# Kernel optimization log

Hardware: AMD Instinct MI355X
Metric: run time of the kernel (lower is better)

Reference implementation:

```python
import jax, jax.numpy as jnp
import numpy as np

B, S, D, P = 16, 128, 768, 1024
N_CLASSES = 121  # dataset != 'restaurant'


def setup_inputs() -> dict:
    key = jax.random.key(0)
    ks = jax.random.split(key, 8)
    scale = lambda fan_in: 1.0 / np.sqrt(fan_in)
    return {
        "spans_embedding": jax.random.normal(ks[0], (B, S, D), dtype=jnp.float32),
        "W1": jax.random.normal(ks[1], (3 * D, 2 * D), dtype=jnp.float32) * scale(3 * D),
        "b1": jnp.zeros((2 * D,), dtype=jnp.float32),
        "W2": jax.random.normal(ks[2], (2 * D, D), dtype=jnp.float32) * scale(2 * D),
        "b2": jnp.zeros((D,), dtype=jnp.float32),
        "W3": jax.random.normal(ks[3], (D, N_CLASSES), dtype=jnp.float32) * scale(D),
        "b3": jnp.zeros((N_CLASSES,), dtype=jnp.float32),
        "span_masks": jnp.ones((B, S), dtype=jnp.int32),
        "batch_idx": jax.random.randint(ks[4], (P,), 0, B, dtype=jnp.int64),
        "aspect_idx": jax.random.randint(ks[5], (P,), 0, S - 2, dtype=jnp.int64),
        "opinion_idx": jax.random.randint(ks[6], (P,), 0, S - 2, dtype=jnp.int64),
    }


def reference(spans_embedding, W1, b1, W2, b2, W3, b3,
              span_masks, batch_idx, aspect_idx, opinion_idx):
    S_ = spans_embedding.shape[1]
    pos = jnp.arange(S_)
    last = jnp.sum(span_masks, axis=1) - 1          # [B] last valid span index
    li = last[batch_idx]                             # [P]
    emb = spans_embedding[batch_idx]                 # [P, S, D] gathered per pair

    def rng_max(lo, hi):                             # max over spans in [lo, hi)
        mask = (pos[None, :] >= lo[:, None]) & (pos[None, :] < hi[:, None])
        return jnp.max(jnp.where(mask[:, :, None], emb, -jnp.inf), axis=1)

    def rng_mean(lo, hi):                            # mean over spans in [lo, hi)
        m = ((pos[None, :] >= lo[:, None]) & (pos[None, :] < hi[:, None])).astype(emb.dtype)
        cnt = jnp.maximum(jnp.sum(m, axis=1), 1.0)
        return jnp.einsum('ps,psd->pd', m, emb) / cnt[:, None]

    ones = jnp.ones_like(aspect_idx)
    # boundary index b: aspect when aspect!=0, else opinion (matches all non-both-zero branches)
    b = jnp.where(aspect_idx != 0, aspect_idx, opinion_idx)
    emb0 = spans_embedding[batch_idx, 0]             # [P, D]
    embL = spans_embedding[batch_idx, li]            # [P, D]
    left_nz = jnp.where((b == 1)[:, None], emb0, rng_max(ones, b))
    right_nz = jnp.where((b == li)[:, None], embL, rng_max(b, li))

    both0 = (aspect_idx == 0) & (opinion_idx == 0)
    left = jnp.where(both0[:, None], rng_mean(ones, li), left_nz)
    right = jnp.where(both0[:, None], rng_max(ones, li), right_nz)

    aspect_rep = spans_embedding[batch_idx, aspect_idx]
    o_eff = jnp.where(opinion_idx == 0, li, opinion_idx)
    opinion_rep = spans_embedding[batch_idx, o_eff]

    x = jnp.concatenate([aspect_rep + opinion_rep, left, right], axis=1)  # [P, 3D]
    h = jax.nn.relu(x @ W1 + b1)
    h = jax.nn.relu(h @ W2 + b2)
    return h @ W3 + b3                               # [P, n_classes]
```

## Files before the change

### kernel.cpp

```cpp
#include <hip/hip_runtime.h>
#include <hip/hip_bf16.h>
#include <math.h>

#define S_LEN 128
#define D_DIM 768
#define P_PAIRS 1024
#define B_BATCH 16

typedef __attribute__((ext_vector_type(8))) short bf16x8;
typedef __attribute__((ext_vector_type(4))) float f32x4;

#define PB_UNITS (B_BATCH * (D_DIM / 64))
#define T1_UNITS ((2304 / 64) * (1536 / 64))
#define T2_UNITS ((1536 / 64) * (768 / 64))
#define T3_UNITS ((768 / 64) * (128 / 64))

union SmemU {
    struct {
        ushort semb[128][64];
        ushort spref[128][64];
        ushort ssuf[128][64];
        ushort smean[64];
        float  lred[3][4][64];
        int    li;
    } pb;
    float t64[64][65];
};

__device__ __forceinline__ ushort f2bf(float f) {
    __hip_bfloat16 h = __float2bfloat16(f);
    return *(ushort*)&h;
}

__device__ __forceinline__ float bf2f(ushort u) {
    unsigned int x = ((unsigned int)u) << 16;
    float f;
    __builtin_memcpy(&f, &x, 4);
    return f;
}

__device__ __forceinline__ void gload16(const void* g, void* l) {
    __builtin_amdgcn_global_load_lds(
        (const __attribute__((address_space(1))) void*)g,
        (__attribute__((address_space(3))) void*)l, 16, 0, 0);
}

__global__ __launch_bounds__(256) void fused_prep_kernel(
    const float* __restrict__ emb_all,
    const int* __restrict__ span_masks,
    const int* __restrict__ batch_idx,
    const int* __restrict__ aspect_idx,
    const int* __restrict__ opinion_idx,
    ushort* __restrict__ X,
    const float* __restrict__ W1, ushort* __restrict__ W1t,
    const float* __restrict__ W2, ushort* __restrict__ W2t,
    const float* __restrict__ W3, ushort* __restrict__ W3t)
{
    __shared__ SmemU sm;
    __shared__ int wsum[4];
    int bid = blockIdx.x;
    int tid = threadIdx.x;

    if (bid < PB_UNITS) {
        int b = bid / (D_DIM / 64);
        int chunk = bid % (D_DIM / 64);
        int lane = tid & 63;
        int g = tid >> 6;
        int r0 = g * 32;
        int col = chunk * 64 + lane;

        {
            int mv = (tid < S_LEN) ? span_masks[b * S_LEN + tid] : 0;
            #pragma unroll
            for (int off = 32; off > 0; off >>= 1)
                mv += __shfl_down(mv, off);
            if (lane == 0) wsum[g] = mv;
            __syncthreads();
            if (tid == 0) sm.pb.li = wsum[0] + wsum[1] + wsum[2] + wsum[3] - 1;
            __syncthreads();
        }
        int li = sm.pb.li;

        const float* embb = emb_all + (size_t)b * S_LEN * D_DIM;

        float v[32];
        #pragma unroll
        for (int r = 0; r < 32; ++r) {
            v[r] = embb[(size_t)(r0 + r) * D_DIM + col];
            sm.pb.semb[r0 + r][lane] = f2bf(v[r]);
        }

        float wmax = -INFINITY, umax = -INFINITY, s = 0.f;
        #pragma unroll
        for (int r = 0; r < 32; ++r) {
            int gr = r0 + r;
            wmax = fmaxf(wmax, (gr == 0) ? -INFINITY : v[r]);
            bool in = (gr >= 1) && (gr < li);
            umax = fmaxf(umax, in ? v[r] : -INFINITY);
            s += in ? v[r] : 0.f;
        }
        sm.pb.lred[0][g][lane] = wmax;
        sm.pb.lred[1][g][lane] = umax;
        sm.pb.lred[2][g][lane] = s;
        __syncthreads();

        float basep = -INFINITY;
        #pragma unroll
        for (int gg = 0; gg < 3; ++gg)
            if (gg < g) basep = fmaxf(basep, sm.pb.lred[0][gg][lane]);
        float bases = -INFINITY;
        #pragma unroll
        for (int gg = 1; gg < 4; ++gg)
            if (gg > g) bases = fmaxf(bases, sm.pb.lred[1][gg][lane]);

        if (g == 0) {
            float tot = sm.pb.lred[2][0][lane] + sm.pb.lred[2][1][lane]
                      + sm.pb.lred[2][2][lane] + sm.pb.lred[2][3][lane];
            int cnt = (li - 1) > 0 ? (li - 1) : 1;
            sm.pb.smean[lane] = f2bf(tot / (float)cnt);
        }

        float m = basep;
        #pragma unroll
        for (int r = 0; r < 32; ++r) {
            int gr = r0 + r;
            m = fmaxf(m, (gr == 0) ? -INFINITY : v[r]);
            sm.pb.spref[gr][lane] = f2bf(m);
        }
        float m2 = bases;
        #pragma unroll
        for (int r = 31; r >= 0; --r) {
            int gr = r0 + r;
            bool in = (gr >= 1) && (gr < li);
            m2 = fmaxf(m2, in ? v[r] : -INFINITY);
            if (gr >= 1) sm.pb.ssuf[gr][lane] = f2bf(m2);
        }
        __syncthreads();

        int pbase = g * 256;
        for (int c = 0; c < 256; c += 64) {
            int p = pbase + c + lane;
            int vb = batch_idx[p];
            int va = aspect_idx[p];
            int vo = opinion_idx[p];
            unsigned long long mask = __ballot(vb == b);
            while (mask) {
                int i = __ffsll((long long)mask) - 1;
                mask &= mask - 1;
                int pp = pbase + c + i;
                int a = __shfl(va, i);
                int o = __shfl(vo, i);
                bool both0 = (a == 0) && (o == 0);
                int bnd = (a != 0) ? a : o;
                int oe = (o == 0) ? li : o;
                float ar  = bf2f(sm.pb.semb[a][lane]);
                float orp = bf2f(sm.pb.semb[oe][lane]);
                ushort left, right;
                if (both0) {
                    left  = sm.pb.smean[lane];
                    right = sm.pb.spref[li - 1][lane];
                } else {
                    left  = (bnd == 1)  ? sm.pb.semb[0][lane]
                                        : sm.pb.spref[bnd - 1][lane];
                    right = (bnd == li) ? sm.pb.semb[li][lane]
                                        : sm.pb.ssuf[bnd][lane];
                }
                size_t base = (size_t)pp * (3 * D_DIM) + col;
                X[base]             = f2bf(ar + orp);
                X[base + D_DIM]     = left;
                X[base + 2 * D_DIM] = right;
            }
        }
    } else {
        int tb = bid - PB_UNITS;
        const float* in; ushort* out; int K, N, Npad, bx, by;
        if (tb < T1_UNITS) {
            in = W1; out = W1t; K = 2304; N = 1536; Npad = 1536;
            bx = tb % (2304 / 64); by = tb / (2304 / 64);
        } else if (tb < T1_UNITS + T2_UNITS) {
            tb -= T1_UNITS;
            in = W2; out = W2t; K = 1536; N = 768; Npad = 768;
            bx = tb % (1536 / 64); by = tb / (1536 / 64);
        } else {
            tb -= T1_UNITS + T2_UNITS;
            in = W3; out = W3t; K = 768; N = 121; Npad = 128;
            bx = tb % (768 / 64); by = tb / (768 / 64);
        }
        int k0 = bx * 64, n0 = by * 64;

        int kr = tid >> 2;
        int nq = (tid & 3) * 16;
        if (n0 + 64 <= N) {
            #pragma unroll
            for (int j = 0; j < 4; ++j) {
                float4 vv = *(const float4*)&in[(size_t)(k0 + kr) * N + n0 + nq + j * 4];
                *(float4*)&sm.t64[kr][nq + j * 4] = vv;
            }
        } else {
            #pragma unroll
            for (int j = 0; j < 16; ++j) {
                int n = n0 + nq + j;
                sm.t64[kr][nq + j] = (n < N) ? in[(size_t)(k0 + kr) * N + n] : 0.f;
            }
        }
        __syncthreads();

        int nr = tid >> 2;
        int kq = (tid & 3) * 16;
        if (n0 + nr < Npad) {
            ushort tmp[16];
            #pragma unroll
            for (int j = 0; j < 16; ++j) tmp[j] = f2bf(sm.t64[kq + j][nr]);
            ushort* dst = out + (size_t)(n0 + nr) * K + k0 + kq;
            *(bf16x8*)dst       = *(bf16x8*)&tmp[0];
            *(bf16x8*)(dst + 8) = *(bf16x8*)&tmp[8];
        }
    }
}

template<int WRITE_BF16, int RELU>
__global__ __launch_bounds__(256, 2) void gemm_mfma(
    const ushort* __restrict__ A,
    const ushort* __restrict__ Bt,
    const float* __restrict__ bias,
    void* __restrict__ Cout,
    int M, int N, int K)
{
    __shared__ ushort lds[4][128 * 64];
    int tid = threadIdx.x;
    int lane = tid & 63;
    int w = tid >> 6;
    int wr = w >> 1, wc = w & 1;
    int rowBase = blockIdx.y * 64;
    int colBase = blockIdx.x * 64;

    int srow  = lane >> 3;
    int scolb = (((lane & 7) ^ srow) << 4);
    const char* Abase = (const char*)(A  + (size_t)rowBase * K);
    const char* Bbase = (const char*)(Bt + (size_t)colBase * K);
    size_t rstride = (size_t)K * 2;

    f32x4 acc[2][2] = {};
    int nt = K >> 6;

    auto stage = [&](int buf, int t) {
        size_t kb0 = (size_t)t << 7;
        #pragma unroll
        for (int i = 0; i < 2; ++i) {
            int r = w * 16 + i * 8 + srow;
            gload16(Abase + (size_t)r * rstride + kb0 + scolb,
                    &lds[buf][(w * 16 + i * 8) * 64]);
        }
        #pragma unroll
        for (int i = 0; i < 2; ++i) {
            int r = w * 16 + i * 8 + srow;
            gload16(Bbase + (size_t)r * rstride + kb0 + scolb,
                    &lds[buf][(64 + w * 16 + i * 8) * 64]);
        }
    };

    stage(0, 0);
    stage(1, 1);
    stage(2, 2);

    for (int t = 0; t < nt; ++t) {
        int cur = t & 3;
        int ahead = nt - 1 - t;
        if (ahead >= 2)      asm volatile("s_waitcnt vmcnt(8)" ::: "memory");
        else if (ahead == 1) asm volatile("s_waitcnt vmcnt(4)" ::: "memory");
        else                 asm volatile("s_waitcnt vmcnt(0)" ::: "memory");
        __builtin_amdgcn_s_barrier();
        __builtin_amdgcn_sched_barrier(0);

        if (t + 3 < nt) stage((t + 3) & 3, t + 3);

        const char* lb = (const char*)&lds[cur][0];
        int kq = (lane >> 4) << 4;
        bf16x8 af[2][2], bfr[2][2];
        #pragma unroll
        for (int m = 0; m < 2; ++m) {
            int row = wr * 32 + m * 16 + (lane & 15);
            #pragma unroll
            for (int kk = 0; kk < 2; ++kk) {
                int addr = row * 128 + ((kq + kk * 64) ^ ((row & 7) << 4));
                af[m][kk] = *(const bf16x8*)(lb + addr);
            }
        }
        #pragma unroll
        for (int n = 0; n < 2; ++n) {
            int row = 64 + wc * 32 + n * 16 + (lane & 15);
            #pragma unroll
            for (int kk = 0; kk < 2; ++kk) {
                int addr = row * 128 + ((kq + kk * 64) ^ ((row & 7) << 4));
                bfr[n][kk] = *(const bf16x8*)(lb + addr);
            }
        }
        __builtin_amdgcn_s_setprio(1);
        #pragma unroll
        for (int m = 0; m < 2; ++m)
            #pragma unroll
            for (int n = 0; n < 2; ++n)
                #pragma unroll
                for (int kk = 0; kk < 2; ++kk)
                    acc[m][n] = __builtin_amdgcn_mfma_f32_16x16x32_bf16(
                        af[m][kk], bfr[n][kk], acc[m][n], 0, 0, 0);
        __builtin_amdgcn_s_setprio(0);
    }

    #pragma unroll
    for (int m = 0; m < 2; ++m) {
        #pragma unroll
        for (int n = 0; n < 2; ++n) {
            #pragma unroll
            for (int j = 0; j < 4; ++j) {
                int row = rowBase + wr * 32 + m * 16 + (lane >> 4) * 4 + j;
                int col = colBase + wc * 32 + n * 16 + (lane & 15);
                if (col < N && row < M) {
                    float v = acc[m][n][j] + bias[col];
                    if (RELU) v = fmaxf(v, 0.f);
                    if (WRITE_BF16)
                        ((ushort*)Cout)[(size_t)row * N + col] = f2bf(v);
                    else
                        ((float*)Cout)[(size_t)row * N + col] = v;
                }
            }
        }
    }
}

extern "C" void kernel_launch(void* const* d_in, const int* in_sizes, int n_in,
                              void* d_out, int out_size, void* d_ws, size_t ws_size,
                              hipStream_t stream) {
    const float* emb        = (const float*)d_in[0];
    const float* W1         = (const float*)d_in[1];
    const float* b1         = (const float*)d_in[2];
    const float* W2         = (const float*)d_in[3];
    const float* b2         = (const float*)d_in[4];
    const float* W3         = (const float*)d_in[5];
    const float* b3         = (const float*)d_in[6];
    const int* span_masks   = (const int*)d_in[7];
    const int* batch_idx    = (const int*)d_in[8];
    const int* aspect_idx   = (const int*)d_in[9];
    const int* opinion_idx  = (const int*)d_in[10];
    float* out = (float*)d_out;

    ushort* Xb  = (ushort*)d_ws;
    ushort* H2  = Xb;
    ushort* W1t = Xb  + (size_t)1024 * 2304;
    ushort* W2t = W1t + (size_t)1536 * 2304;
    ushort* W3t = W2t + (size_t)768 * 1536;
    ushort* H1  = W3t + (size_t)128 * 768;

    fused_prep_kernel<<<PB_UNITS + T1_UNITS + T2_UNITS + T3_UNITS, 256, 0, stream>>>(
        emb, span_masks, batch_idx, aspect_idx, opinion_idx, Xb,
        W1, W1t, W2, W2t, W3, W3t);

    gemm_mfma<1,1><<<dim3(1536/64, 1024/64), 256, 0, stream>>>(Xb, W1t, b1, H1, 1024, 1536, 2304);
    gemm_mfma<1,1><<<dim3( 768/64, 1024/64), 256, 0, stream>>>(H1, W2t, b2, H2, 1024, 768, 1536);
    gemm_mfma<0,0><<<dim3( 128/64, 1024/64), 256, 0, stream>>>(H2, W3t, b3, out, 1024, 121, 768);
}
```

Measured before the change: 54.10 us.

## Split prep kernel and overlap W2/W3 transposes with first GEMM

The single fused prep launch is split into a span-feature kernel and a separate W1 transpose kernel. The W2 and W3 transpose blocks are appended to the first GEMM's grid so they run alongside the GEMM tiles instead of before them. The aim is to shorten the serial prep phase by moving work the first GEMM does not need off its critical path. The cost is one extra launch and a GEMM1 kernel whose shared memory is a union sized by the GEMM buffers.

```diff
diff --git a/kernel.cpp b/kernel.cpp
--- a/kernel.cpp
+++ b/kernel.cpp
@@ -14,17 +14,20 @@
 #define T1_UNITS ((2304 / 64) * (1536 / 64))
 #define T2_UNITS ((1536 / 64) * (768 / 64))
 #define T3_UNITS ((768 / 64) * (128 / 64))
-
-union SmemU {
-    struct {
-        ushort semb[128][64];
-        ushort spref[128][64];
-        ushort ssuf[128][64];
-        ushort smean[64];
-        float  lred[3][4][64];
-        int    li;
-    } pb;
-    float t64[64][65];
+#define G1_TILES (24 * 16)
+
+struct SmemPB {
+    ushort semb[128][64];
+    ushort spref[128][64];
+    ushort ssuf[128][64];
+    ushort smean[64];
+    float  lred[3][4][64];
+    int    li;
+};
+
+union GSmem {
+    ushort lds[4][128 * 64];
+    float  t64[64][65];
 };
 
 __device__ __forceinline__ ushort f2bf(float f) {
@@ -43,6 +46,41 @@
     __builtin_amdgcn_global_load_lds(
         (const __attribute__((address_space(1))) void*)g,
         (__attribute__((address_space(3))) void*)l, 16, 0, 0);
+}
+
+__device__ __forceinline__ void transpose_unit(
+    float (*t64)[65], const float* __restrict__ in, ushort* __restrict__ out,
+    int K, int N, int Npad, int bx, int by, int tid)
+{
+    int k0 = bx * 64, n0 = by * 64;
+
+    int kr = tid >> 2;
+    int nq = (tid & 3) * 16;
+    if (n0 + 64 <= N) {
+        #pragma unroll
+        for (int j = 0; j < 4; ++j) {
+            float4 vv = *(const float4*)&in[(size_t)(k0 + kr) * N + n0 + nq + j * 4];
+            *(float4*)&t64[kr][nq + j * 4] = vv;
+        }
+    } else {
+        #pragma unroll
+        for (int j = 0; j < 16; ++j) {
+            int n = n0 + nq + j;
+            t64[kr][nq + j] = (n < N) ? in[(size_t)(k0 + kr) * N + n] : 0.f;
+        }
+    }
+    __syncthreads();
+
+    int nr = tid >> 2;
+    int kq = (tid & 3) * 16;
+    if (n0 + nr < Npad) {
+        ushort tmp[16];
+        #pragma unroll
+        for (int j = 0; j < 16; ++j) tmp[j] = f2bf(t64[kq + j][nr]);
+        ushort* dst = out + (size_t)(n0 + nr) * K + k0 + kq;
+        *(bf16x8*)dst       = *(bf16x8*)&tmp[0];
+        *(bf16x8*)(dst + 8) = *(bf16x8*)&tmp[8];
+    }
 }
 
 __global__ __launch_bounds__(256) void fused_prep_kernel(
@@ -51,169 +89,247 @@
     const int* __restrict__ batch_idx,
     const int* __restrict__ aspect_idx,
     const int* __restrict__ opinion_idx,
-    ushort* __restrict__ X,
-    const float* __restrict__ W1, ushort* __restrict__ W1t,
+    ushort* __restrict__ X)
+{
+    __shared__ SmemPB sm;
+    __shared__ int wsum[4];
+    int bid = blockIdx.x;
+    int tid = threadIdx.x;
+
+    int b = bid / (D_DIM / 64);
+    int chunk = bid % (D_DIM / 64);
+    int lane = tid & 63;
+    int g = tid >> 6;
+    int r0 = g * 32;
+    int col = chunk * 64 + lane;
+
+    {
+        int mv = (tid < S_LEN) ? span_masks[b * S_LEN + tid] : 0;
+        #pragma unroll
+        for (int off = 32; off > 0; off >>= 1)
+            mv += __shfl_down(mv, off);
+        if (lane == 0) wsum[g] = mv;
+        __syncthreads();
+        if (tid == 0) sm.li = wsum[0] + wsum[1] + wsum[2] + wsum[3] - 1;
+        __syncthreads();
+    }
+    int li = sm.li;
+
+    const float* embb = emb_all + (size_t)b * S_LEN * D_DIM;
+
+    float v[32];
+    #pragma unroll
+    for (int r = 0; r < 32; ++r) {
+        v[r] = embb[(size_t)(r0 + r) * D_DIM + col];
+        sm.semb[r0 + r][lane] = f2bf(v[r]);
+    }
+
+    float wmax = -INFINITY, umax = -INFINITY, s = 0.f;
+    #pragma unroll
+    for (int r = 0; r < 32; ++r) {
+        int gr = r0 + r;
+        wmax = fmaxf(wmax, (gr == 0) ? -INFINITY : v[r]);
+        bool in = (gr >= 1) && (gr < li);
+        umax = fmaxf(umax, in ? v[r] : -INFINITY);
+        s += in ? v[r] : 0.f;
+    }
+    sm.lred[0][g][lane] = wmax;
+    sm.lred[1][g][lane] = umax;
+    sm.lred[2][g][lane] = s;
+    __syncthreads();
+
+    float basep = -INFINITY;
+    #pragma unroll
+    for (int gg = 0; gg < 3; ++gg)
+        if (gg < g) basep = fmaxf(basep, sm.lred[0][gg][lane]);
+    float bases = -INFINITY;
+    #pragma unroll
+    for (int gg = 1; gg < 4; ++gg)
+        if (gg > g) bases = fmaxf(bases, sm.lred[1][gg][lane]);
+
+    if (g == 0) {
+        float tot = sm.lred[2][0][lane] + sm.lred[2][1][lane]
+                  + sm.lred[2][2][lane] + sm.lred[2][3][lane];
+        int cnt = (li - 1) > 0 ? (li - 1) : 1;
+        sm.smean[lane] = f2bf(tot / (float)cnt);
+    }
+
+    float m = basep;
+    #pragma unroll
+    for (int r = 0; r < 32; ++r) {
+        int gr = r0 + r;
+        m = fmaxf(m, (gr == 0) ? -INFINITY : v[r]);
+        sm.spref[gr][lane] = f2bf(m);
+    }
+    float m2 = bases;
+    #pragma unroll
+    for (int r = 31; r >= 0; --r) {
+        int gr = r0 + r;
+        bool in = (gr >= 1) && (gr < li);
+        m2 = fmaxf(m2, in ? v[r] : -INFINITY);
+        if (gr >= 1) sm.ssuf[gr][lane] = f2bf(m2);
+    }
+    __syncthreads();
+
+    int pbase = g * 256;
+    for (int c = 0; c < 256; c += 64) {
+        int p = pbase + c + lane;
+        int vb = batch_idx[p];
+        int va = aspect_idx[p];
+        int vo = opinion_idx[p];
+        unsigned long long mask = __ballot(vb == b);
+        while (mask) {
+            int i = __ffsll((long long)mask) - 1;
+            mask &= mask - 1;
+            int pp = pbase + c + i;
+            int a = __shfl(va, i);
+            int o = __shfl(vo, i);
+            bool both0 = (a == 0) && (o == 0);
+            int bnd = (a != 0) ? a : o;
+            int oe = (o == 0) ? li : o;
+            float ar  = bf2f(sm.semb[a][lane]);
+            float orp = bf2f(sm.semb[oe][lane]);
+            ushort left, right;
+            if (both0) {
+                left  = sm.smean[lane];
+                right = sm.spref[li - 1][lane];
+            } else {
+                left  = (bnd == 1)  ? sm.semb[0][lane]
+                                    : sm.spref[bnd - 1][lane];
+                right = (bnd == li) ? sm.semb[li][lane]
+                                    : sm.ssuf[bnd][lane];
+            }
+            size_t base = (size_t)pp * (3 * D_DIM) + col;
+            X[base]             = f2bf(ar + orp);
+            X[base + D_DIM]     = left;
+            X[base + 2 * D_DIM] = right;
+        }
+    }
+}
+
+__global__ __launch_bounds__(256) void w1_transpose_kernel(
+    const float* __restrict__ W1, ushort* __restrict__ W1t)
+{
+    __shared__ float t64[64][65];
+    int tb = blockIdx.x;
+    transpose_unit(t64, W1, W1t, 2304, 1536, 1536, tb % 36, tb / 36, threadIdx.x);
+}
+
+__global__ __launch_bounds__(256, 2) void gemm1_plus_t23(
+    const ushort* __restrict__ A,
+    const ushort* __restrict__ Bt,
+    const float* __restrict__ bias,
+    ushort* __restrict__ Cout,
     const float* __restrict__ W2, ushort* __restrict__ W2t,
     const float* __restrict__ W3, ushort* __restrict__ W3t)
 {
-    __shared__ SmemU sm;
-    __shared__ int wsum[4];
+    constexpr int M = 1024, N = 1536, K = 2304;
+    __shared__ GSmem gs;
     int bid = blockIdx.x;
     int tid = threadIdx.x;
 
-    if (bid < PB_UNITS) {
-        int b = bid / (D_DIM / 64);
-        int chunk = bid % (D_DIM / 64);
-        int lane = tid & 63;
-        int g = tid >> 6;
-        int r0 = g * 32;
-        int col = chunk * 64 + lane;
-
-        {
-            int mv = (tid < S_LEN) ? span_masks[b * S_LEN + tid] : 0;
-            #pragma unroll
-            for (int off = 32; off > 0; off >>= 1)
-                mv += __shfl_down(mv, off);
-            if (lane == 0) wsum[g] = mv;
-            __syncthreads();
-            if (tid == 0) sm.pb.li = wsum[0] + wsum[1] + wsum[2] + wsum[3] - 1;
-            __syncthreads();
-        }
-        int li = sm.pb.li;
-
-        const float* embb = emb_all + (size_t)b * S_LEN * D_DIM;
-
-        float v[32];
-        #pragma unroll
-        for (int r = 0; r < 32; ++r) {
-            v[r] = embb[(size_t)(r0 + r) * D_DIM + col];
-            sm.pb.semb[r0 + r][lane] = f2bf(v[r]);
-        }
-
-        float wmax = -INFINITY, umax = -INFINITY, s = 0.f;
-        #pragma unroll
-        for (int r = 0; r < 32; ++r) {
-            int gr = r0 + r;
-            wmax = fmaxf(wmax, (gr == 0) ? -INFINITY : v[r]);
-            bool in = (gr >= 1) && (gr < li);
-            umax = fmaxf(umax, in ? v[r] : -INFINITY);
-            s += in ? v[r] : 0.f;
-        }
-        sm.pb.lred[0][g][lane] = wmax;
-        sm.pb.lred[1][g][lane] = umax;
-        sm.pb.lred[2][g][lane] = s;
-        __syncthreads();
-
-        float basep = -INFINITY;
-        #pragma unroll
-        for (int gg = 0; gg < 3; ++gg)
-            if (gg < g) basep = fmaxf(basep, sm.pb.lred[0][gg][lane]);
-        float bases = -INFINITY;
-        #pragma unroll
-        for (int gg = 1; gg < 4; ++gg)
-            if (gg > g) bases = fmaxf(bases, sm.pb.lred[1][gg][lane]);
-
-        if (g == 0) {
-            float tot = sm.pb.lred[2][0][lane] + sm.pb.lred[2][1][lane]
-                      + sm.pb.lred[2][2][lane] + sm.pb.lred[2][3][lane];
-            int cnt = (li - 1) > 0 ? (li - 1) : 1;
-            sm.pb.smean[lane] = f2bf(tot / (float)cnt);
-        }
-
-        float m = basep;
-        #pragma unroll
-        for (int r = 0; r < 32; ++r) {
-            int gr = r0 + r;
-            m = fmaxf(m, (gr == 0) ? -INFINITY : v[r]);
-            sm.pb.spref[gr][lane] = f2bf(m);
-        }
-        float m2 = bases;
-        #pragma unroll
-        for (int r = 31; r >= 0; --r) {
-            int gr = r0 + r;
-            bool in = (gr >= 1) && (gr < li);
-            m2 = fmaxf(m2, in ? v[r] : -INFINITY);
-            if (gr >= 1) sm.pb.ssuf[gr][lane] = f2bf(m2);
-        }
-        __syncthreads();
-
-        int pbase = g * 256;
-        for (int c = 0; c < 256; c += 64) {
-            int p = pbase + c + lane;
-            int vb = batch_idx[p];
-            int va = aspect_idx[p];
-            int vo = opinion_idx[p];
-            unsigned long long mask = __ballot(vb == b);
-            while (mask) {
-                int i = __ffsll((long long)mask) - 1;
-                mask &= mask - 1;
-                int pp = pbase + c + i;
-                int a = __shfl(va, i);
-                int o = __shfl(vo, i);
-                bool both0 = (a == 0) && (o == 0);
-                int bnd = (a != 0) ? a : o;
-                int oe = (o == 0) ? li : o;
-                float ar  = bf2f(sm.pb.semb[a][lane]);
-                float orp = bf2f(sm.pb.semb[oe][lane]);
-                ushort left, right;
-                if (both0) {
-                    left  = sm.pb.smean[lane];
-                    right = sm.pb.spref[li - 1][lane];
-                } else {
-                    left  = (bnd == 1)  ? sm.pb.semb[0][lane]
-                                        : sm.pb.spref[bnd - 1][lane];
-                    right = (bnd == li) ? sm.pb.semb[li][lane]
-                                        : sm.pb.ssuf[bnd][lane];
-                }
-                size_t base = (size_t)pp * (3 * D_DIM) + col;
-                X[base]             = f2bf(ar + orp);
-                X[base + D_DIM]     = left;
-                X[base + 2 * D_DIM] = right;
-            }
-        }
-    } else {
-        int tb = bid - PB_UNITS;
-        const float* in; ushort* out; int K, N, Npad, bx, by;
-        if (tb < T1_UNITS) {
-            in = W1; out = W1t; K = 2304; N = 1536; Npad = 1536;
-            bx = tb % (2304 / 64); by = tb / (2304 / 64);
-        } else if (tb < T1_UNITS + T2_UNITS) {
-            tb -= T1_UNITS;
-            in = W2; out = W2t; K = 1536; N = 768; Npad = 768;
-            bx = tb % (1536 / 64); by = tb / (1536 / 64);
-        } else {
-            tb -= T1_UNITS + T2_UNITS;
-            in = W3; out = W3t; K = 768; N = 121; Npad = 128;
-            bx = tb % (768 / 64); by = tb / (768 / 64);
-        }
-        int k0 = bx * 64, n0 = by * 64;
-
-        int kr = tid >> 2;
-        int nq = (tid & 3) * 16;
-        if (n0 + 64 <= N) {
+    if (bid >= G1_TILES) {
+        int tb = bid - G1_TILES;
+        if (tb < T2_UNITS)
+            transpose_unit(gs.t64, W2, W2t, 1536, 768, 768, tb % 24, tb / 24, tid);
+        else {
+            tb -= T2_UNITS;
+            transpose_unit(gs.t64, W3, W3t, 768, 121, 128, tb % 12, tb / 12, tid);
+        }
+        return;
+    }
+
+    int lane = tid & 63;
+    int w = tid >> 6;
+    int wr = w >> 1, wc = w & 1;
+    int bx = bid % 24, by = bid / 24;
+    int rowBase = by * 64;
+    int colBase = bx * 64;
+
+    int srow  = lane >> 3;
+    int scolb = (((lane & 7) ^ srow) << 4);
+    const char* Abase = (const char*)(A  + (size_t)rowBase * K);
+    const char* Bbase = (const char*)(Bt + (size_t)colBase * K);
+    size_t rstride = (size_t)K * 2;
+
+    f32x4 acc[2][2] = {};
+    int nt = K >> 6;
+
+    auto stage = [&](int buf, int t) {
+        size_t kb0 = (size_t)t << 7;
+        #pragma unroll
+        for (int i = 0; i < 2; ++i) {
+            int r = w * 16 + i * 8 + srow;
+            gload16(Abase + (size_t)r * rstride + kb0 + scolb,
+                    &gs.lds[buf][(w * 16 + i * 8) * 64]);
+        }
+        #pragma unroll
+        for (int i = 0; i < 2; ++i) {
+            int r = w * 16 + i * 8 + srow;
+            gload16(Bbase + (size_t)r * rstride + kb0 + scolb,
+                    &gs.lds[buf][(64 + w * 16 + i * 8) * 64]);
+        }
+    };
+
+    stage(0, 0);
+    stage(1, 1);
+    stage(2, 2);
+
+    for (int t = 0; t < nt; ++t) {
+        int cur = t & 3;
+        int ahead = nt - 1 - t;
+        if (ahead >= 2)      asm volatile("s_waitcnt vmcnt(8)" ::: "memory");
+        else if (ahead == 1) asm volatile("s_waitcnt vmcnt(4)" ::: "memory");
+        else                 asm volatile("s_waitcnt vmcnt(0)" ::: "memory");
+        __builtin_amdgcn_s_barrier();
+        __builtin_amdgcn_sched_barrier(0);
+
+        if (t + 3 < nt) stage((t + 3) & 3, t + 3);
+
+        const char* lb = (const char*)&gs.lds[cur][0];
+        int kq = (lane >> 4) << 4;
+        bf16x8 af[2][2], bfr[2][2];
+        #pragma unroll
+        for (int m = 0; m < 2; ++m) {
+            int row = wr * 32 + m * 16 + (lane & 15);
+            #pragma unroll
+            for (int kk = 0; kk < 2; ++kk) {
+                int addr = row * 128 + ((kq + kk * 64) ^ ((row & 7) << 4));
+                af[m][kk] = *(const bf16x8*)(lb + addr);
+            }
+        }
+        #pragma unroll
+        for (int n = 0; n < 2; ++n) {
+            int row = 64 + wc * 32 + n * 16 + (lane & 15);
+            #pragma unroll
+            for (int kk = 0; kk < 2; ++kk) {
+                int addr = row * 128 + ((kq + kk * 64) ^ ((row & 7) << 4));
+                bfr[n][kk] = *(const bf16x8*)(lb + addr);
+            }
+        }
+        __builtin_amdgcn_s_setprio(1);
+        #pragma unroll
+        for (int m = 0; m < 2; ++m)
+            #pragma unroll
+            for (int n = 0; n < 2; ++n)
+                #pragma unroll
+                for (int kk = 0; kk < 2; ++kk)
+                    acc[m][n] = __builtin_amdgcn_mfma_f32_16x16x32_bf16(
+                        af[m][kk], bfr[n][kk], acc[m][n], 0, 0, 0);
+        __builtin_amdgcn_s_setprio(0);
+    }
+
+    #pragma unroll
+    for (int m = 0; m < 2; ++m) {
+        #pragma unroll
+        for (int n = 0; n < 2; ++n) {
             #pragma unroll
             for (int j = 0; j < 4; ++j) {
-                float4 vv = *(const float4*)&in[(size_t)(k0 + kr) * N + n0 + nq + j * 4];
-                *(float4*)&sm.t64[kr][nq + j * 4] = vv;
-            }
-        } else {
-            #pragma unroll
-            for (int j = 0; j < 16; ++j) {
-                int n = n0 + nq + j;
-                sm.t64[kr][nq + j] = (n < N) ? in[(size_t)(k0 + kr) * N + n] : 0.f;
-            }
-        }
-        __syncthreads();
-
-        int nr = tid >> 2;
-        int kq = (tid & 3) * 16;
-        if (n0 + nr < Npad) {
-            ushort tmp[16];
-            #pragma unroll
-            for (int j = 0; j < 16; ++j) tmp[j] = f2bf(sm.t64[kq + j][nr]);
-            ushort* dst = out + (size_t)(n0 + nr) * K + k0 + kq;
-            *(bf16x8*)dst       = *(bf16x8*)&tmp[0];
-            *(bf16x8*)(dst + 8) = *(bf16x8*)&tmp[8];
+                int row = rowBase + wr * 32 + m * 16 + (lane >> 4) * 4 + j;
+                int col = colBase + wc * 32 + n * 16 + (lane & 15);
+                float v = fmaxf(acc[m][n][j] + bias[col], 0.f);
+                Cout[(size_t)row * N + col] = f2bf(v);
+            }
         }
     }
 }
@@ -351,11 +467,13 @@
     ushort* W3t = W2t + (size_t)768 * 1536;
     ushort* H1  = W3t + (size_t)128 * 768;
 
-    fused_prep_kernel<<<PB_UNITS + T1_UNITS + T2_UNITS + T3_UNITS, 256, 0, stream>>>(
-        emb, span_masks, batch_idx, aspect_idx, opinion_idx, Xb,
-        W1, W1t, W2, W2t, W3, W3t);
-
-    gemm_mfma<1,1><<<dim3(1536/64, 1024/64), 256, 0, stream>>>(Xb, W1t, b1, H1, 1024, 1536, 2304);
+    fused_prep_kernel<<<PB_UNITS, 256, 0, stream>>>(
+        emb, span_masks, batch_idx, aspect_idx, opinion_idx, Xb);
+    w1_transpose_kernel<<<T1_UNITS, 256, 0, stream>>>(W1, W1t);
+
+    gemm1_plus_t23<<<G1_TILES + T2_UNITS + T3_UNITS, 256, 0, stream>>>(
+        Xb, W1t, b1, H1, W2, W2t, W3, W3t);
+
     gemm_mfma<1,1><<<dim3( 768/64, 1024/64), 256, 0, stream>>>(H1, W2t, b2, H2, 1024, 768, 1536);
     gemm_mfma<0,0><<<dim3( 128/64, 1024/64), 256, 0, stream>>>(H2, W3t, b3, out, 1024, 121, 768);
 }
```

Measured after the change: 56.00 us. 1.04x slower.
